# Kernel optimization log

Hardware: AMD Instinct MI355X
Metric: run time of the kernel (lower is better)

The kernel has to match this reference:

```python
import jax, jax.numpy as jnp
import numpy as np

NEG_SLOPE = 0.2


def gat_conv(x, src, dst, W, att_src, att_dst, bias, heads, out_ch, concat):
    """PyG-style GATConv (eval mode, self-loops already appended to src/dst)."""
    N = x.shape[0]
    h = (x @ W).reshape(N, heads, out_ch)                      # [N,H,C]
    a_src = jnp.einsum('nhc,hc->nh', h, att_src)               # [N,H]
    a_dst = jnp.einsum('nhc,hc->nh', h, att_dst)               # [N,H]
    e = jax.nn.leaky_relu(a_src[src] + a_dst[dst], NEG_SLOPE)  # [E,H]
    # numerically-stable softmax segmented by destination node
    emax = jax.ops.segment_max(e, dst, num_segments=N)         # [N,H]
    e = jnp.exp(e - emax[dst])
    denom = jax.ops.segment_sum(e, dst, num_segments=N)
    alpha = e / (denom[dst] + 1e-16)                           # [E,H]
    msg = h[src] * alpha[..., None]                            # [E,H,C]
    out = jax.ops.segment_sum(msg, dst, num_segments=N)        # [N,H,C]
    out = out.reshape(N, heads * out_ch) if concat else out.mean(axis=1)
    return out + bias


def setup_inputs() -> dict:
    key = jax.random.key(0)
    ks = jax.random.split(key, 9)
    N, E, IN, OUT = 100000, 1600000, 128, 40
    H1, C1 = 8, 8
    x = jax.random.normal(ks[0], (N, IN), dtype=jnp.float32)
    edge_index = jax.random.randint(ks[1], (2, E), 0, N, dtype=jnp.int64)
    s = 0.1
    return {
        'x': x,
        'edge_index': edge_index,
        'W1': jax.random.normal(ks[2], (IN, H1 * C1), dtype=jnp.float32) * s,
        'att_src1': jax.random.normal(ks[3], (H1, C1), dtype=jnp.float32) * s,
        'att_dst1': jax.random.normal(ks[4], (H1, C1), dtype=jnp.float32) * s,
        'b1': jnp.zeros((H1 * C1,), dtype=jnp.float32),
        'W2': jax.random.normal(ks[5], (H1 * C1, OUT), dtype=jnp.float32) * s,
        'att_src2': jax.random.normal(ks[6], (1, OUT), dtype=jnp.float32) * s,
        'att_dst2': jax.random.normal(ks[7], (1, OUT), dtype=jnp.float32) * s,
        'b2': jnp.zeros((OUT,), dtype=jnp.float32),
    }


def reference(x, edge_index, W1, att_src1, att_dst1, b1, W2, att_src2, att_dst2, b2):
    N = x.shape[0]
    loops = jnp.arange(N, dtype=edge_index.dtype)
    src = jnp.concatenate([edge_index[0], loops])  # self-loops (PyG default)
    dst = jnp.concatenate([edge_index[1], loops])
    h = gat_conv(x, src, dst, W1, att_src1, att_dst1, b1, 8, 8, True)
    h = jax.nn.elu(h)  # dropout is identity in eval mode
    out = gat_conv(h, src, dst, W2, att_src2, att_dst2, b2, 1, W2.shape[1], False)
    return jax.nn.log_softmax(out, axis=-1)
```

## Files before the change

kernel.cpp:

```cpp
#include <hip/hip_runtime.h>
#include <math.h>

#define NEG_SLOPE 0.2f
#define BSHIFT 8
#define MAXBUK 512

typedef __attribute__((ext_vector_type(8))) short short8;
typedef __attribute__((ext_vector_type(4))) float floatx4;

static __device__ __forceinline__ float lrelu_exp(float e) {
    e = fmaxf(e, NEG_SLOPE * e);
    return __expf(e);
}

static __device__ __forceinline__ short f2bf(float f) {
    union { float f; unsigned u; } v; v.f = f;
    unsigned r = v.u + 0x7FFFu + ((v.u >> 16) & 1u);
    return (short)(r >> 16);
}
static __device__ __forceinline__ float bf2f(unsigned short s) {
    union { float f; unsigned u; } v;
    v.u = ((unsigned)s) << 16;
    return v.f;
}
static __device__ __forceinline__ float bfpair_lo(unsigned v) {
    union { float f; unsigned u; } x; x.u = v << 16; return x.f;
}
static __device__ __forceinline__ float bfpair_hi(unsigned v) {
    union { float f; unsigned u; } x; x.u = v & 0xffff0000u; return x.f;
}
static __device__ __forceinline__ void splitbf(float f, short& hi, short& lo) {
    hi = f2bf(f);
    lo = f2bf(f - bf2f((unsigned short)hi));
}


__global__ __launch_bounds__(512) void k_hist(const int* __restrict__ dst, int E, int CHUNK,
                                              int NBLK, int NBUK, int* __restrict__ blockhist) {
    __shared__ int hist[MAXBUK];
    int t = threadIdx.x, b = blockIdx.x;
    for (int i = t; i < NBUK; i += 512) hist[i] = 0;
    __syncthreads();
    int e0 = b * CHUNK, e1 = e0 + CHUNK; if (e1 > E) e1 = E;
    for (int e = e0 + t; e < e1; e += 512) atomicAdd(&hist[dst[e] >> BSHIFT], 1);
    __syncthreads();
    for (int i = t; i < NBUK; i += 512) blockhist[(size_t)i * NBLK + b] = hist[i];
}

__global__ __launch_bounds__(256) void k_colscan(int* __restrict__ blockhist,
                                                 int* __restrict__ btot, int NBLK) {
    int bucket = blockIdx.x, t = threadIdx.x;
    int lane = t & 63, wv = t >> 6;
    __shared__ int wsum[4];
    __shared__ int carry_s;
    if (t == 0) carry_s = 0;
    __syncthreads();
    for (int base = 0; base < NBLK; base += 256) {
        int idx = base + t;
        int v = (idx < NBLK) ? blockhist[(size_t)bucket * NBLK + idx] : 0;
        int s = v;
#pragma unroll
        for (int o = 1; o < 64; o <<= 1) {
            int u = __shfl_up(s, o, 64);
            if (lane >= o) s += u;
        }
        if (lane == 63) wsum[wv] = s;
        __syncthreads();
        int b0 = 0;
#pragma unroll
        for (int w = 0; w < 4; ++w) b0 += (w < wv) ? wsum[w] : 0;
        int excl = s + b0 - v + carry_s;
        if (idx < NBLK) blockhist[(size_t)bucket * NBLK + idx] = excl;
        __syncthreads();
        if (t == 255) carry_s += s + b0;
        __syncthreads();
    }
    if (t == 0) btot[bucket] = carry_s;
}

__global__ __launch_bounds__(512) void k_bucket_scan(const int* __restrict__ btot,
                                                     int* __restrict__ bucketbase, int NBUK) {
    __shared__ int sh[512];
    int t = threadIdx.x;
    int v = (t < NBUK) ? btot[t] : 0;
    sh[t] = v;
    __syncthreads();
#pragma unroll
    for (int o = 1; o < 512; o <<= 1) {
        int u = (t >= o) ? sh[t - o] : 0;
        __syncthreads();
        sh[t] += u;
        __syncthreads();
    }
    if (t < NBUK) bucketbase[t] = sh[t] - v;
    if (t == NBUK - 1) bucketbase[NBUK] = sh[t];
}

__global__ __launch_bounds__(512) void k_partition(const int* __restrict__ src,
                                                   const int* __restrict__ dst, int E, int CHUNK,
                                                   int NBLK, int NBUK,
                                                   const int* __restrict__ blockhist,
                                                   const int* __restrict__ bucketbase,
                                                   unsigned* __restrict__ packed) {
    __shared__ int cur[MAXBUK];
    int t = threadIdx.x, b = blockIdx.x;
    for (int i = t; i < NBUK; i += 512)
        cur[i] = blockhist[(size_t)i * NBLK + b] + bucketbase[i];
    __syncthreads();
    int e0 = b * CHUNK, e1 = e0 + CHUNK; if (e1 > E) e1 = E;
    for (int e = e0 + t; e < e1; e += 512) {
        int d = dst[e], s = src[e];
        int pos = atomicAdd(&cur[d >> BSHIFT], 1);
        packed[pos] = ((unsigned)s << 8) | ((unsigned)d & 255u);
    }
}

__global__ __launch_bounds__(256) void k_fine(const unsigned* __restrict__ packed,
                                              const int* __restrict__ bucketbase,
                                              int* __restrict__ offsets,
                                              int* __restrict__ csr_src,
                                              int N, int NBUK) {
    __shared__ int fcnt[256];
    __shared__ int wsum[4];
    int bucket = blockIdx.x, t = threadIdx.x;
    int lo = bucket << BSHIFT;
    int nn = N - lo; if (nn > 256) nn = 256;
    int ebase = bucketbase[bucket];
    int ecnt = bucketbase[bucket + 1] - ebase;
    fcnt[t] = 0;
    __syncthreads();
    for (int i = t; i < ecnt; i += 256) {
        unsigned p = packed[ebase + i];
        atomicAdd(&fcnt[p & 255u], 1);
    }
    __syncthreads();
    int v = fcnt[t];
    int lane = t & 63, wv = t >> 6;
    int s = v;
#pragma unroll
    for (int o = 1; o < 64; o <<= 1) {
        int u = __shfl_up(s, o, 64);
        if (lane >= o) s += u;
    }
    if (lane == 63) wsum[wv] = s;
    __syncthreads();
    int base = 0;
#pragma unroll
    for (int w = 0; w < 4; ++w) base += (w < wv) ? wsum[w] : 0;
    int excl = s + base - v;
    if (t < nn) offsets[lo + t] = ebase + excl;
    if (bucket == NBUK - 1 && t == 0) offsets[N] = ebase + ecnt;
    __syncthreads();
    fcnt[t] = excl;
    __syncthreads();
    for (int i = t; i < ecnt; i += 256) {
        unsigned p = packed[ebase + i];
        int pos = atomicAdd(&fcnt[p & 255u], 1);
        csr_src[ebase + pos] = (int)(p >> 8);
    }
}

__global__ __launch_bounds__(256) void k_splitW2(const float* __restrict__ W2,
                                                 short* __restrict__ w2h,
                                                 short* __restrict__ w2l) {
    int i = blockIdx.x * 256 + threadIdx.x;
    if (i < 64 * 48) {
        int row = i / 48, col = i % 48;
        short hi = 0, lo = 0;
        if (col < 40) splitbf(W2[row * 40 + col], hi, lo);
        w2h[i] = hi; w2l[i] = lo;
    }
}

__global__ __launch_bounds__(256) void k_gemm1(const float* __restrict__ x,
                                               const float* __restrict__ W1,
                                               const float* __restrict__ att_s,
                                               const float* __restrict__ att_d,
                                               unsigned short* __restrict__ h1b,
                                               float* __restrict__ a_s1,
                                               float* __restrict__ a_d1, int N) {
    int tid = threadIdx.x, wave = tid >> 6, lane = tid & 63;
    int n16 = lane & 15, q = lane >> 4;
    int nb = blockIdx.x * 64 + wave * 16;
    if (nb >= N) return;

    short8 bfr[4][4];
#pragma unroll
    for (int ct = 0; ct < 4; ++ct) {
        int n = ct * 16 + n16;
#pragma unroll
        for (int kc = 0; kc < 4; ++kc) {
            int k0 = kc * 32 + q * 8;
            short8 b;
#pragma unroll
            for (int j = 0; j < 8; ++j) b[j] = f2bf(W1[(k0 + j) * 64 + n]);
            bfr[ct][kc] = b;
        }
    }

    int arow = nb + n16; if (arow >= N) arow = N - 1;
    const float* xr = x + (size_t)arow * 128 + q * 8;
    short8 afr[4];
#pragma unroll
    for (int kc = 0; kc < 4; ++kc) {
        float4 u0 = *(const float4*)(xr + kc * 32);
        float4 u1 = *(const float4*)(xr + kc * 32 + 4);
        short8 a;
        a[0] = f2bf(u0.x); a[1] = f2bf(u0.y); a[2] = f2bf(u0.z); a[3] = f2bf(u0.w);
        a[4] = f2bf(u1.x); a[5] = f2bf(u1.y); a[6] = f2bf(u1.z); a[7] = f2bf(u1.w);
        afr[kc] = a;
    }

    floatx4 acc[4];
#pragma unroll
    for (int ct = 0; ct < 4; ++ct) {
        floatx4 c = {0.f, 0.f, 0.f, 0.f};
#pragma unroll
        for (int kc = 0; kc < 4; ++kc)
            c = __builtin_amdgcn_mfma_f32_16x16x32_bf16(afr[kc], bfr[ct][kc], c, 0, 0, 0);
        acc[ct] = c;
    }

#pragma unroll
    for (int ct = 0; ct < 4; ++ct) {
#pragma unroll
        for (int r = 0; r < 4; ++r) {
            int row = nb + q * 4 + r;
            if (row < N) h1b[(size_t)row * 64 + ct * 16 + n16] = (unsigned short)f2bf(acc[ct][r]);
        }
    }

#pragma unroll
    for (int ct = 0; ct < 4; ++ct) {
        float as = att_s[ct * 16 + n16];
        float ad = att_d[ct * 16 + n16];
#pragma unroll
        for (int r = 0; r < 4; ++r) {
            float ps = acc[ct][r] * as;
            float pd = acc[ct][r] * ad;
#pragma unroll
            for (int m = 1; m < 8; m <<= 1) {
                ps += __shfl_xor(ps, m, 64);
                pd += __shfl_xor(pd, m, 64);
            }
            int row = nb + q * 4 + r;
            if ((n16 & 7) == 0 && row < N) {
                int h = 2 * ct + (n16 >> 3);
                a_s1[row * 8 + h] = ps;
                a_d1[row * 8 + h] = pd;
            }
        }
    }
}

__global__ __launch_bounds__(256) void k_agg1(const unsigned short* __restrict__ h1b,
                                              const float* __restrict__ a_s1,
                                              const float* __restrict__ a_d1,
                                              const int* __restrict__ offsets,
                                              const int* __restrict__ csr_src,
                                              const float* __restrict__ b1,
                                              float* __restrict__ y1, int N) {
    int wave = threadIdx.x >> 6, lane = threadIdx.x & 63;
    int d = blockIdx.x * 4 + wave;
    if (d >= N) return;
    int g = lane >> 3;
    int h = lane & 7;
    float ad = a_d1[d * 8 + h];
    float acc[8] = {0.f, 0.f, 0.f, 0.f, 0.f, 0.f, 0.f, 0.f};
    float wsum_l = 0.f;
    if (g == 0) {
        float w0 = lrelu_exp(a_s1[d * 8 + h] + ad);
        uint4 v = *(const uint4*)(h1b + (size_t)d * 64 + 8 * h);
        acc[0] = w0 * bfpair_lo(v.x); acc[1] = w0 * bfpair_hi(v.x);
        acc[2] = w0 * bfpair_lo(v.y); acc[3] = w0 * bfpair_hi(v.y);
        acc[4] = w0 * bfpair_lo(v.z); acc[5] = w0 * bfpair_hi(v.z);
        acc[6] = w0 * bfpair_lo(v.w); acc[7] = w0 * bfpair_hi(v.w);
        wsum_l = w0;
    }
    int i0 = offsets[d], i1 = offsets[d + 1];
    for (int base = i0; base < i1; base += 64) {
        int m = i1 - base; if (m > 64) m = 64;
        int sv = (lane < m) ? csr_src[base + lane] : 0;
        for (int j = 0; j < m; j += 16) {
            int eA = j + g;
            int siA = __shfl(sv, eA, 64);
            bool liveB = (j + 8 < m);
            if (liveB) {
                int eB = j + 8 + g;
                int siB = __shfl(sv, eB, 64);
                float evA = a_s1[siA * 8 + h] + ad;
                float evB = a_s1[siB * 8 + h] + ad;
                uint4 vA = *(const uint4*)(h1b + (size_t)siA * 64 + 8 * h);
                uint4 vB = *(const uint4*)(h1b + (size_t)siB * 64 + 8 * h);
                float wA = (eA < m) ? lrelu_exp(evA) : 0.f;
                float wB = (eB < m) ? lrelu_exp(evB) : 0.f;
                wsum_l += wA + wB;
                acc[0] = fmaf(wA, bfpair_lo(vA.x), acc[0]);
                acc[1] = fmaf(wA, bfpair_hi(vA.x), acc[1]);
                acc[2] = fmaf(wA, bfpair_lo(vA.y), acc[2]);
                acc[3] = fmaf(wA, bfpair_hi(vA.y), acc[3]);
                acc[4] = fmaf(wA, bfpair_lo(vA.z), acc[4]);
                acc[5] = fmaf(wA, bfpair_hi(vA.z), acc[5]);
                acc[6] = fmaf(wA, bfpair_lo(vA.w), acc[6]);
                acc[7] = fmaf(wA, bfpair_hi(vA.w), acc[7]);
                acc[0] = fmaf(wB, bfpair_lo(vB.x), acc[0]);
                acc[1] = fmaf(wB, bfpair_hi(vB.x), acc[1]);
                acc[2] = fmaf(wB, bfpair_lo(vB.y), acc[2]);
                acc[3] = fmaf(wB, bfpair_hi(vB.y), acc[3]);
                acc[4] = fmaf(wB, bfpair_lo(vB.z), acc[4]);
                acc[5] = fmaf(wB, bfpair_hi(vB.z), acc[5]);
                acc[6] = fmaf(wB, bfpair_lo(vB.w), acc[6]);
                acc[7] = fmaf(wB, bfpair_hi(vB.w), acc[7]);
            } else {
                float evA = a_s1[siA * 8 + h] + ad;
                uint4 vA = *(const uint4*)(h1b + (size_t)siA * 64 + 8 * h);
                float wA = (eA < m) ? lrelu_exp(evA) : 0.f;
                wsum_l += wA;
                acc[0] = fmaf(wA, bfpair_lo(vA.x), acc[0]);
                acc[1] = fmaf(wA, bfpair_hi(vA.x), acc[1]);
                acc[2] = fmaf(wA, bfpair_lo(vA.y), acc[2]);
                acc[3] = fmaf(wA, bfpair_hi(vA.y), acc[3]);
                acc[4] = fmaf(wA, bfpair_lo(vA.z), acc[4]);
                acc[5] = fmaf(wA, bfpair_hi(vA.z), acc[5]);
                acc[6] = fmaf(wA, bfpair_lo(vA.w), acc[6]);
                acc[7] = fmaf(wA, bfpair_hi(vA.w), acc[7]);
            }
        }
    }
#pragma unroll
    for (int mm = 8; mm < 64; mm <<= 1) {
#pragma unroll
        for (int k = 0; k < 8; ++k) acc[k] += __shfl_xor(acc[k], mm, 64);
        wsum_l += __shfl_xor(wsum_l, mm, 64);
    }
    if (g == 0) {
        float inv = 1.f / (wsum_l + 1e-16f);
        float4 bA = *(const float4*)(b1 + 8 * h);
        float4 bB = *(const float4*)(b1 + 8 * h + 4);
        float o[8];
        o[0] = acc[0] * inv + bA.x;
        o[1] = acc[1] * inv + bA.y;
        o[2] = acc[2] * inv + bA.z;
        o[3] = acc[3] * inv + bA.w;
        o[4] = acc[4] * inv + bB.x;
        o[5] = acc[5] * inv + bB.y;
        o[6] = acc[6] * inv + bB.z;
        o[7] = acc[7] * inv + bB.w;
#pragma unroll
        for (int k = 0; k < 8; ++k) o[k] = o[k] > 0.f ? o[k] : (__expf(o[k]) - 1.f);
        float4 s0 = make_float4(o[0], o[1], o[2], o[3]);
        float4 s1 = make_float4(o[4], o[5], o[6], o[7]);
        *(float4*)(y1 + (size_t)d * 64 + 8 * h) = s0;
        *(float4*)(y1 + (size_t)d * 64 + 8 * h + 4) = s1;
    }
}

__global__ __launch_bounds__(256) void k_gemm2(const float* __restrict__ y1,
                                               const short* __restrict__ w2h,
                                               const short* __restrict__ w2l,
                                               const float* __restrict__ att_s,
                                               const float* __restrict__ att_d,
                                               unsigned short* __restrict__ h2b,
                                               float* __restrict__ a2s,
                                               float* __restrict__ a2d, int N) {
    int tid = threadIdx.x, wave = tid >> 6, lane = tid & 63;
    int n16 = lane & 15, q = lane >> 4;
    int nb = blockIdx.x * 64 + wave * 16;
    if (nb >= N) return;

    int arow = nb + n16; if (arow >= N) arow = N - 1;
    const float* yr = y1 + (size_t)arow * 64 + q * 8;
    short8 ah[2], al[2];
#pragma unroll
    for (int kc = 0; kc < 2; ++kc) {
        float4 u0 = *(const float4*)(yr + kc * 32);
        float4 u1 = *(const float4*)(yr + kc * 32 + 4);
        short8 h, l; short hi, lo;
        splitbf(u0.x, hi, lo); h[0] = hi; l[0] = lo;
        splitbf(u0.y, hi, lo); h[1] = hi; l[1] = lo;
        splitbf(u0.z, hi, lo); h[2] = hi; l[2] = lo;
        splitbf(u0.w, hi, lo); h[3] = hi; l[3] = lo;
        splitbf(u1.x, hi, lo); h[4] = hi; l[4] = lo;
        splitbf(u1.y, hi, lo); h[5] = hi; l[5] = lo;
        splitbf(u1.z, hi, lo); h[6] = hi; l[6] = lo;
        splitbf(u1.w, hi, lo); h[7] = hi; l[7] = lo;
        ah[kc] = h; al[kc] = l;
    }

    float psr[4] = {0.f, 0.f, 0.f, 0.f}, pdr[4] = {0.f, 0.f, 0.f, 0.f};
#pragma unroll
    for (int ct = 0; ct < 3; ++ct) {
        int n = ct * 16 + n16;
        short8 bh0, bh1, bl0, bl1;
#pragma unroll
        for (int j = 0; j < 8; ++j) {
            int k0 = q * 8 + j;
            bh0[j] = w2h[k0 * 48 + n];
            bl0[j] = w2l[k0 * 48 + n];
            bh1[j] = w2h[(32 + k0) * 48 + n];
            bl1[j] = w2l[(32 + k0) * 48 + n];
        }
        floatx4 c = {0.f, 0.f, 0.f, 0.f};
        c = __builtin_amdgcn_mfma_f32_16x16x32_bf16(ah[0], bl0, c, 0, 0, 0);
        c = __builtin_amdgcn_mfma_f32_16x16x32_bf16(al[0], bh0, c, 0, 0, 0);
        c = __builtin_amdgcn_mfma_f32_16x16x32_bf16(ah[0], bh0, c, 0, 0, 0);
        c = __builtin_amdgcn_mfma_f32_16x16x32_bf16(ah[1], bl1, c, 0, 0, 0);
        c = __builtin_amdgcn_mfma_f32_16x16x32_bf16(al[1], bh1, c, 0, 0, 0);
        c = __builtin_amdgcn_mfma_f32_16x16x32_bf16(ah[1], bh1, c, 0, 0, 0);

        int col = ct * 16 + n16;
#pragma unroll
        for (int r = 0; r < 4; ++r) {
            int row = nb + q * 4 + r;
            if (col < 40 && row < N) h2b[(size_t)row * 40 + col] = (unsigned short)f2bf(c[r]);
        }
        float asv = (col < 40) ? att_s[col] : 0.f;
        float adv = (col < 40) ? att_d[col] : 0.f;
#pragma unroll
        for (int r = 0; r < 4; ++r) {
            psr[r] = fmaf(c[r], asv, psr[r]);
            pdr[r] = fmaf(c[r], adv, pdr[r]);
        }
    }
#pragma unroll
    for (int r = 0; r < 4; ++r) {
        float ps = psr[r], pd = pdr[r];
#pragma unroll
        for (int m = 1; m < 16; m <<= 1) {
            ps += __shfl_xor(ps, m, 64);
            pd += __shfl_xor(pd, m, 64);
        }
        int row = nb + q * 4 + r;
        if (n16 == 0 && row < N) { a2s[row] = ps; a2d[row] = pd; }
    }
}

__global__ __launch_bounds__(256) void k_agg2(const unsigned short* __restrict__ h2b,
                                              const float* __restrict__ a2s,
                                              const float* __restrict__ a2d,
                                              const int* __restrict__ offsets,
                                              const int* __restrict__ csr_src,
                                              const float* __restrict__ b2,
                                              float* __restrict__ out, int N) {
    int wave = threadIdx.x >> 6, lane = threadIdx.x & 63;
    int d = blockIdx.x * 4 + wave;
    if (d >= N) return;
    int t = lane / 20;
    int c = lane % 20;
    float ad = a2d[d];
    float w0 = lrelu_exp(a2s[d] + ad);
    float accx = 0.f, accy = 0.f;
    if (t == 0) {
        unsigned v = *(const unsigned*)(h2b + (size_t)d * 40 + 2 * c);
        accx = w0 * bfpair_lo(v);
        accy = w0 * bfpair_hi(v);
    }
    float wsum_l = 0.f;
    int i0 = offsets[d], i1 = offsets[d + 1];
    for (int base = i0; base < i1; base += 48) {
        int m = i1 - base; if (m > 48) m = 48;
        int sv = 0; float wv = 0.f;
        if (lane < m) {
            sv = csr_src[base + lane];
            wv = lrelu_exp(a2s[sv] + ad);
        }
        wsum_l += wv;
        for (int j = 0; j < m; j += 24) {
            int si[8]; float wq[8]; unsigned vv[8];
#pragma unroll
            for (int u = 0; u < 8; ++u) {
                int e = j + 3 * u + t;
                si[u] = __shfl(sv, e, 64);
                wq[u] = __shfl(wv, e, 64);
            }
#pragma unroll
            for (int u = 0; u < 8; ++u)
                vv[u] = *(const unsigned*)(h2b + (size_t)si[u] * 40 + 2 * c);
#pragma unroll
            for (int u = 0; u < 8; ++u) {
                accx = fmaf(wq[u], bfpair_lo(vv[u]), accx);
                accy = fmaf(wq[u], bfpair_hi(vv[u]), accy);
            }
        }
    }
    accx += __shfl(accx, lane + 20, 64) + __shfl(accx, lane + 40, 64);
    accy += __shfl(accy, lane + 20, 64) + __shfl(accy, lane + 40, 64);
#pragma unroll
    for (int mm = 1; mm < 64; mm <<= 1) wsum_l += __shfl_xor(wsum_l, mm, 64);
    float wsum = wsum_l + w0;
    bool act = (lane < 20);
    float inv = 1.f / (wsum + 1e-16f);
    float ox = act ? (accx * inv + b2[2 * c]) : -INFINITY;
    float oy = act ? (accy * inv + b2[2 * c + 1]) : -INFINITY;
    float mx = fmaxf(ox, oy);
#pragma unroll
    for (int mm = 1; mm < 64; mm <<= 1) mx = fmaxf(mx, __shfl_xor(mx, mm, 64));
    float ex = act ? (__expf(ox - mx) + __expf(oy - mx)) : 0.f;
#pragma unroll
    for (int mm = 1; mm < 64; mm <<= 1) ex += __shfl_xor(ex, mm, 64);
    if (act) {
        float lse = __logf(ex);
        float2 o2 = make_float2(ox - mx - lse, oy - mx - lse);
        *(float2*)(out + (size_t)d * 40 + 2 * c) = o2;
    }
}


extern "C" void kernel_launch(void* const* d_in, const int* in_sizes, int n_in,
                              void* d_out, int out_size, void* d_ws, size_t ws_size,
                              hipStream_t stream) {
    const float* x   = (const float*)d_in[0];
    const int*   ei  = (const int*)d_in[1];
    const float* W1  = (const float*)d_in[2];
    const float* as1 = (const float*)d_in[3];
    const float* ad1 = (const float*)d_in[4];
    const float* b1  = (const float*)d_in[5];
    const float* W2  = (const float*)d_in[6];
    const float* as2 = (const float*)d_in[7];
    const float* ad2 = (const float*)d_in[8];
    const float* b2  = (const float*)d_in[9];
    float* out = (float*)d_out;

    int N = in_sizes[0] / 128;
    int E = in_sizes[1] / 2;
    const int* src = ei;
    const int* dst = ei + E;

    int NBUK = (N + 255) >> BSHIFT;
    int CHUNK = 4096;
    int NBLK = (E + CHUNK - 1) / CHUNK;

    char* ws = (char*)d_ws;
    size_t off = 0;
    auto alloc = [&](size_t bytes) -> char* {
        char* p = ws + off;
        off += (bytes + 255) & ~(size_t)255;
        return p;
    };
    unsigned short* h1b = (unsigned short*)alloc((size_t)N * 64 * 2);
    float* a_s1    = (float*)alloc((size_t)N * 8 * 4);
    float* a_d1    = (float*)alloc((size_t)N * 8 * 4);
    float* y1      = (float*)alloc((size_t)N * 64 * 4);
    size_t shared_sz = (size_t)N * 40 * 2;
    if ((size_t)E * 4 > shared_sz) shared_sz = (size_t)E * 4;
    char*  region  = alloc(shared_sz);
    unsigned short* h2b = (unsigned short*)region;
    unsigned* packed    = (unsigned*)region;
    float* a2s     = (float*)alloc((size_t)N * 4);
    float* a2d     = (float*)alloc((size_t)N * 4);
    int*   offsets = (int*)alloc((size_t)(N + 1) * 4);
    int*   csr_src = (int*)alloc((size_t)E * 4);
    int*   blockhist  = (int*)alloc((size_t)NBUK * NBLK * 4);
    int*   btot       = (int*)alloc((size_t)NBUK * 4);
    int*   bucketbase = (int*)alloc((size_t)(NBUK + 1) * 4);
    short* w2h     = (short*)alloc((size_t)64 * 48 * 2);
    short* w2l     = (short*)alloc((size_t)64 * 48 * 2);

    int nb = (N + 3) / 4;
    int gb = (N + 63) / 64;

    k_hist<<<NBLK, 512, 0, stream>>>(dst, E, CHUNK, NBLK, NBUK, blockhist);
    k_colscan<<<NBUK, 256, 0, stream>>>(blockhist, btot, NBLK);
    k_bucket_scan<<<1, 512, 0, stream>>>(btot, bucketbase, NBUK);
    k_partition<<<NBLK, 512, 0, stream>>>(src, dst, E, CHUNK, NBLK, NBUK, blockhist,
                                          bucketbase, packed);
    k_fine<<<NBUK, 256, 0, stream>>>(packed, bucketbase, offsets, csr_src, N, NBUK);
    k_splitW2<<<12, 256, 0, stream>>>(W2, w2h, w2l);
    k_gemm1<<<gb, 256, 0, stream>>>(x, W1, as1, ad1, h1b, a_s1, a_d1, N);
    k_agg1<<<nb, 256, 0, stream>>>(h1b, a_s1, a_d1, offsets, csr_src, b1, y1, N);
    k_gemm2<<<gb, 256, 0, stream>>>(y1, w2h, w2l, as2, ad2, h2b, a2s, a2d, N);
    k_agg2<<<nb, 256, 0, stream>>>(h2b, a2s, a2d, offsets, csr_src, b2, out, N);
}
```

Baseline: 192.0 us.

## Gather layer-2 features with 16-byte loads across 12 edge groups per wave

Restructures the second-layer aggregation so each lane loads 8 bf16 channels with one 16-byte load. The wave now handles 12 edges at once (5 lanes per edge) instead of 3 edges with 20 lanes of 4-byte loads, and edge chunks grow from 48 to 60. The goal is fewer, wider gather instructions and more edges in flight per wave. In exchange it needs a longer cross-group shuffle reduction over 8 accumulators, and 4 of the 64 lanes sit idle.

```diff
diff --git a/kernel.cpp b/kernel.cpp
--- a/kernel.cpp
+++ b/kernel.cpp
@@ -445,20 +445,23 @@
     int wave = threadIdx.x >> 6, lane = threadIdx.x & 63;
     int d = blockIdx.x * 4 + wave;
     if (d >= N) return;
-    int t = lane / 20;
-    int c = lane % 20;
+    bool act = (lane < 60);
+    int g = act ? (lane / 5) : 0;
+    int c = act ? (lane - g * 5) : 0;
     float ad = a2d[d];
     float w0 = lrelu_exp(a2s[d] + ad);
-    float accx = 0.f, accy = 0.f;
-    if (t == 0) {
-        unsigned v = *(const unsigned*)(h2b + (size_t)d * 40 + 2 * c);
-        accx = w0 * bfpair_lo(v);
-        accy = w0 * bfpair_hi(v);
+    float acc[8] = {0.f, 0.f, 0.f, 0.f, 0.f, 0.f, 0.f, 0.f};
+    if (lane < 5) {
+        uint4 v = *(const uint4*)(h2b + (size_t)d * 40 + 8 * c);
+        acc[0] = w0 * bfpair_lo(v.x); acc[1] = w0 * bfpair_hi(v.x);
+        acc[2] = w0 * bfpair_lo(v.y); acc[3] = w0 * bfpair_hi(v.y);
+        acc[4] = w0 * bfpair_lo(v.z); acc[5] = w0 * bfpair_hi(v.z);
+        acc[6] = w0 * bfpair_lo(v.w); acc[7] = w0 * bfpair_hi(v.w);
     }
     float wsum_l = 0.f;
     int i0 = offsets[d], i1 = offsets[d + 1];
-    for (int base = i0; base < i1; base += 48) {
-        int m = i1 - base; if (m > 48) m = 48;
+    for (int base = i0; base < i1; base += 60) {
+        int m = i1 - base; if (m > 60) m = 60;
         int sv = 0; float wv = 0.f;
         if (lane < m) {
             sv = csr_src[base + lane];
@@ -466,42 +469,89 @@
         }
         wsum_l += wv;
         for (int j = 0; j < m; j += 24) {
-            int si[8]; float wq[8]; unsigned vv[8];
-#pragma unroll
-            for (int u = 0; u < 8; ++u) {
-                int e = j + 3 * u + t;
-                si[u] = __shfl(sv, e, 64);
-                wq[u] = __shfl(wv, e, 64);
+            int eA = j + g;
+            int siA = __shfl(sv, eA, 64);
+            float wqA = __shfl(wv, eA, 64);
+            if (!act || eA >= m) wqA = 0.f;
+            bool liveB = (j + 12 < m);
+            if (liveB) {
+                int eB = j + 12 + g;
+                int siB = __shfl(sv, eB, 64);
+                float wqB = __shfl(wv, eB, 64);
+                if (!act || eB >= m) wqB = 0.f;
+                uint4 vA = *(const uint4*)(h2b + (size_t)siA * 40 + 8 * c);
+                uint4 vB = *(const uint4*)(h2b + (size_t)siB * 40 + 8 * c);
+                acc[0] = fmaf(wqA, bfpair_lo(vA.x), acc[0]);
+                acc[1] = fmaf(wqA, bfpair_hi(vA.x), acc[1]);
+                acc[2] = fmaf(wqA, bfpair_lo(vA.y), acc[2]);
+                acc[3] = fmaf(wqA, bfpair_hi(vA.y), acc[3]);
+                acc[4] = fmaf(wqA, bfpair_lo(vA.z), acc[4]);
+                acc[5] = fmaf(wqA, bfpair_hi(vA.z), acc[5]);
+                acc[6] = fmaf(wqA, bfpair_lo(vA.w), acc[6]);
+                acc[7] = fmaf(wqA, bfpair_hi(vA.w), acc[7]);
+                acc[0] = fmaf(wqB, bfpair_lo(vB.x), acc[0]);
+                acc[1] = fmaf(wqB, bfpair_hi(vB.x), acc[1]);
+                acc[2] = fmaf(wqB, bfpair_lo(vB.y), acc[2]);
+                acc[3] = fmaf(wqB, bfpair_hi(vB.y), acc[3]);
+                acc[4] = fmaf(wqB, bfpair_lo(vB.z), acc[4]);
+                acc[5] = fmaf(wqB, bfpair_hi(vB.z), acc[5]);
+                acc[6] = fmaf(wqB, bfpair_lo(vB.w), acc[6]);
+                acc[7] = fmaf(wqB, bfpair_hi(vB.w), acc[7]);
+            } else {
+                uint4 vA = *(const uint4*)(h2b + (size_t)siA * 40 + 8 * c);
+                acc[0] = fmaf(wqA, bfpair_lo(vA.x), acc[0]);
+                acc[1] = fmaf(wqA, bfpair_hi(vA.x), acc[1]);
+                acc[2] = fmaf(wqA, bfpair_lo(vA.y), acc[2]);
+                acc[3] = fmaf(wqA, bfpair_hi(vA.y), acc[3]);
+                acc[4] = fmaf(wqA, bfpair_lo(vA.z), acc[4]);
+                acc[5] = fmaf(wqA, bfpair_hi(vA.z), acc[5]);
+                acc[6] = fmaf(wqA, bfpair_lo(vA.w), acc[6]);
+                acc[7] = fmaf(wqA, bfpair_hi(vA.w), acc[7]);
             }
-#pragma unroll
-            for (int u = 0; u < 8; ++u)
-                vv[u] = *(const unsigned*)(h2b + (size_t)si[u] * 40 + 2 * c);
-#pragma unroll
-            for (int u = 0; u < 8; ++u) {
-                accx = fmaf(wq[u], bfpair_lo(vv[u]), accx);
-                accy = fmaf(wq[u], bfpair_hi(vv[u]), accy);
-            }
-        }
-    }
-    accx += __shfl(accx, lane + 20, 64) + __shfl(accx, lane + 40, 64);
-    accy += __shfl(accy, lane + 20, 64) + __shfl(accy, lane + 40, 64);
+        }
+    }
+#pragma unroll
+    for (int k = 0; k < 8; ++k) {
+        acc[k] += __shfl(acc[k], lane + 30, 64);
+        acc[k] += __shfl(acc[k], lane + 15, 64);
+        acc[k] += __shfl(acc[k], lane + 5, 64) + __shfl(acc[k], lane + 10, 64);
+    }
 #pragma unroll
     for (int mm = 1; mm < 64; mm <<= 1) wsum_l += __shfl_xor(wsum_l, mm, 64);
     float wsum = wsum_l + w0;
-    bool act = (lane < 20);
+    bool act5 = (lane < 5);
     float inv = 1.f / (wsum + 1e-16f);
-    float ox = act ? (accx * inv + b2[2 * c]) : -INFINITY;
-    float oy = act ? (accy * inv + b2[2 * c + 1]) : -INFINITY;
-    float mx = fmaxf(ox, oy);
-#pragma unroll
-    for (int mm = 1; mm < 64; mm <<= 1) mx = fmaxf(mx, __shfl_xor(mx, mm, 64));
-    float ex = act ? (__expf(ox - mx) + __expf(oy - mx)) : 0.f;
-#pragma unroll
-    for (int mm = 1; mm < 64; mm <<= 1) ex += __shfl_xor(ex, mm, 64);
-    if (act) {
-        float lse = __logf(ex);
-        float2 o2 = make_float2(ox - mx - lse, oy - mx - lse);
-        *(float2*)(out + (size_t)d * 40 + 2 * c) = o2;
+    float o[8];
+    float4 bA = *(const float4*)(b2 + 8 * c);
+    float4 bB = *(const float4*)(b2 + 8 * c + 4);
+    o[0] = acc[0] * inv + bA.x;
+    o[1] = acc[1] * inv + bA.y;
+    o[2] = acc[2] * inv + bA.z;
+    o[3] = acc[3] * inv + bA.w;
+    o[4] = acc[4] * inv + bB.x;
+    o[5] = acc[5] * inv + bB.y;
+    o[6] = acc[6] * inv + bB.z;
+    o[7] = acc[7] * inv + bB.w;
+    float mxl = -INFINITY;
+    if (act5) {
+        mxl = fmaxf(fmaxf(fmaxf(o[0], o[1]), fmaxf(o[2], o[3])),
+                    fmaxf(fmaxf(o[4], o[5]), fmaxf(o[6], o[7])));
+    }
+#pragma unroll
+    for (int mm = 1; mm < 8; mm <<= 1) mxl = fmaxf(mxl, __shfl_xor(mxl, mm, 64));
+    float exl = 0.f;
+    if (act5) {
+#pragma unroll
+        for (int k = 0; k < 8; ++k) exl += __expf(o[k] - mxl);
+    }
+#pragma unroll
+    for (int mm = 1; mm < 8; mm <<= 1) exl += __shfl_xor(exl, mm, 64);
+    if (act5) {
+        float lse = mxl + __logf(exl);
+        float4 s0 = make_float4(o[0] - lse, o[1] - lse, o[2] - lse, o[3] - lse);
+        float4 s1 = make_float4(o[4] - lse, o[5] - lse, o[6] - lse, o[7] - lse);
+        *(float4*)(out + (size_t)d * 40 + 8 * c) = s0;
+        *(float4*)(out + (size_t)d * 40 + 8 * c + 4) = s1;
     }
 }
 
```

New measurement: 192.7 us. About the same (+0.4%).
